# Performance work log

Measured on AMD Instinct MI355X. Metric: run time of the kernel, lower is better.

Reference implementation:

```python
import jax, jax.numpy as jnp
import numpy as np

# LE-like radial basis config (hypers: type='le', r_cut=5.0, mlp=True, no alchemical)
N_MAX_L = [22, 19, 16, 13]      # n_max per angular channel l
L_MAX = len(N_MAX_L) - 1
N_TOTAL = sum(N_MAX_L)          # 70
N_SPECIES = 4                   # all_species = [0,1,2,3]
N_GRID = 1024                   # spline control points
R_CUT = 5.0
HIDDEN = 32                     # hard-coded MLP width in the module
N_EDGES = 400_000


def setup_inputs() -> dict:
    key = jax.random.key(0)
    ks = jax.random.split(key, 7)
    # neighbor distances in [0, r_cut)
    r = jax.random.uniform(ks[0], (N_EDGES,), dtype=jnp.float32) * R_CUT
    neighbor_species = jax.random.randint(ks[1], (N_EDGES,), 0, N_SPECIES)
    # spline table standing in for the precomputed spliner coefficients
    spline_table = jax.random.normal(ks[2], (N_GRID, N_TOTAL), dtype=jnp.float32)
    nmax = max(N_MAX_L)
    sc_in = 1.0 / np.sqrt(nmax)
    sc_h = 1.0 / np.sqrt(HIDDEN)
    # per-(l, species) expert MLP weights, padded to nmax along the n_max_l axis;
    # torch Linear(n_in, n_out, bias=False) == x @ W with W: [n_in, n_out]
    W1 = jax.random.normal(ks[3], (L_MAX + 1, N_SPECIES, nmax, HIDDEN), dtype=jnp.float32) * sc_in
    W2 = jax.random.normal(ks[4], (L_MAX + 1, N_SPECIES, HIDDEN, HIDDEN), dtype=jnp.float32) * sc_h
    W3 = jax.random.normal(ks[5], (L_MAX + 1, N_SPECIES, HIDDEN, HIDDEN), dtype=jnp.float32) * sc_h
    W4 = jax.random.normal(ks[6], (L_MAX + 1, N_SPECIES, HIDDEN, nmax), dtype=jnp.float32) * sc_h
    return {"r": r, "neighbor_species": neighbor_species, "spline_table": spline_table,
            "W1": W1, "W2": W2, "W3": W3, "W4": W4}


def _spline_eval(r, spline_table):
    # linear-interpolation spline over a uniform grid on [0, R_CUT]
    dx = R_CUT / (N_GRID - 1)
    xi = r / dx
    idx = jnp.clip(jnp.floor(xi).astype(jnp.int32), 0, N_GRID - 2)
    frac = (xi - idx.astype(xi.dtype))[:, None]
    return spline_table[idx] * (1.0 - frac) + spline_table[idx + 1] * frac  # [E, N_TOTAL]


def reference(r, neighbor_species, spline_table, W1, W2, W3, W4):
    # 1) spline basis eval: r -> radial_functions [E, N_TOTAL]
    rf = _spline_eval(r, spline_table)
    silu = jax.nn.silu
    outs = []
    off = 0
    # 2) split by n_max_l; per-species expert MLP with scatter-back.
    # Vectorized as: run each species' tiny MLP on all edges, select via mask
    # (equivalent math to the original's nonzero/index_select gather-scatter).
    for l, n_l in enumerate(N_MAX_L):
        x_l = rf[:, off:off + n_l]  # [E, n_l]
        off += n_l
        out_l = jnp.zeros_like(x_l)
        for s in range(N_SPECIES):
            h = silu(x_l @ W1[l, s, :n_l])        # [E, 32]
            h = silu(h @ W2[l, s])                # [E, 32]
            h = silu(h @ W3[l, s])                # [E, 32]
            y = h @ W4[l, s][:, :n_l]             # [E, n_l]
            out_l = jnp.where(neighbor_species[:, None] == s, y, out_l)
        outs.append(out_l)
    # original returns a list split by l; concatenate for a single output array
    return jnp.concatenate(outs, axis=1)  # [E, N_TOTAL]
```

## Files before the change

kernel.cpp:

```cpp
#include <hip/hip_runtime.h>
#include <math.h>

#define BLK 256
#define BX 192
#define TSL 24608

typedef __attribute__((ext_vector_type(8))) short short8;
typedef __attribute__((ext_vector_type(4))) float f32x4;

union Frag {
  short8 s;
  unsigned int u[4];
};

__device__ __forceinline__ unsigned int pack_pair(float a, float b) {
  const unsigned int ua = __float_as_uint(a) + 0x8000u;
  const unsigned int ub = __float_as_uint(b) + 0x8000u;
  return (ua >> 16) | (ub & 0xFFFF0000u);
}

__device__ __forceinline__ void split_pair(float a, float b, unsigned int& hi,
                                           unsigned int& lo) {
  hi = pack_pair(a, b);
  const float ra = a - __uint_as_float(hi << 16);
  const float rb = b - __uint_as_float(hi & 0xFFFF0000u);
  lo = pack_pair(ra, rb);
}

__device__ __forceinline__ f32x4 silu4(f32x4 v) {
#pragma unroll
  for (int i = 0; i < 4; i++) {
    const float e = __builtin_amdgcn_exp2f(v[i] * -1.44269504f);
    v[i] = v[i] * __builtin_amdgcn_rcpf(1.0f + e);
  }
  return v;
}


__global__ void k_zero(int* __restrict__ cnt) {
  if (threadIdx.x < 4) cnt[threadIdx.x] = 0;
}

__global__ void __launch_bounds__(BLK) k_hist(const int* __restrict__ spc, int n,
                                              int* __restrict__ cnt) {
  __shared__ int h[4];
  if (threadIdx.x < 4) h[threadIdx.x] = 0;
  __syncthreads();
  const int i = blockIdx.x * BLK + threadIdx.x;
  if (i < n) atomicAdd(&h[spc[i]], 1);
  __syncthreads();
  if (threadIdx.x < 4) atomicAdd(&cnt[threadIdx.x], h[threadIdx.x]);
}

__global__ void k_prefix(const int* __restrict__ cnt, int* __restrict__ cnt2,
                         int* __restrict__ csum) {
  if (threadIdx.x == 0) {
    int a = 0;
#pragma unroll
    for (int s = 0; s < 4; s++) {
      csum[s] = a;
      cnt2[s] = a;
      a += cnt[s];
    }
  }
}

__global__ void __launch_bounds__(BLK) k_compact(const int* __restrict__ spc,
                                                 const float* __restrict__ r, int n,
                                                 int nb, int* __restrict__ cnt2,
                                                 float* __restrict__ fracs,
                                                 int* __restrict__ toffA,
                                                 int* __restrict__ perm,
                                                 const float* __restrict__ tbl,
                                                 float* __restrict__ wt) {
  if (blockIdx.x >= nb) {
    const int t = (blockIdx.x - nb) * BLK + threadIdx.x;
    if (t < 4 * 1024 * 24) {
      const int l = t / (1024 * 24);
      const int rem = t - l * (1024 * 24);
      const int idx = rem / 24;
      const int j = rem - idx * 24;
      const int off = (l == 0) ? 0 : (l == 1) ? 22 : (l == 2) ? 41 : 57;
      const int nl = (l == 0) ? 22 : (l == 1) ? 19 : (l == 2) ? 16 : 13;
      const float v = (j < nl) ? tbl[idx * 70 + off + j] : 0.f;
      wt[l * TSL + idx * 24 + j] = v;
    }
    if (t < 4 * 32) {
      const int l = t >> 5, j = t & 31;
      wt[l * TSL + 1024 * 24 + j] = 0.f;
    }
    return;
  }

  __shared__ int wcnt[4][4];
  __shared__ int wbase[4][4];
  const int tid = threadIdx.x;
  const int i = blockIdx.x * BLK + tid;
  const int lane = tid & 63;
  const int w = tid >> 6;
  const int s = (i < n) ? spc[i] : -1;
  const float rr = (i < n) ? r[i] : 0.f;

  int rank = 0;
#pragma unroll
  for (int sp = 0; sp < 4; sp++) {
    unsigned long long m = __ballot(s == sp);
    if (lane == 0) wcnt[w][sp] = __popcll(m);
    if (s == sp) rank = __popcll(m & ((1ULL << lane) - 1ULL));
  }
  __syncthreads();
  if (tid < 4) {
    const int c0 = wcnt[0][tid], c1 = wcnt[1][tid], c2 = wcnt[2][tid], c3 = wcnt[3][tid];
    const int b = atomicAdd(&cnt2[tid], c0 + c1 + c2 + c3);
    wbase[0][tid] = b;
    wbase[1][tid] = b + c0;
    wbase[2][tid] = b + c0 + c1;
    wbase[3][tid] = b + c0 + c1 + c2;
  }
  __syncthreads();
  if (s >= 0) {
    const int sp = wbase[w][s] + rank;
    const float xi = rr * (1023.0f / 5.0f);
    int idx = (int)floorf(xi);
    idx = idx < 0 ? 0 : (idx > 1022 ? 1022 : idx);
    fracs[sp] = xi - (float)idx;
    toffA[sp] = idx * 96;
    perm[sp] = i;
  }
}


__device__ __forceinline__ void layer_hl(const Frag* A, const Frag& bh,
                                         const Frag& bl, f32x4& d0, f32x4& d1) {
  f32x4 z = {0.f, 0.f, 0.f, 0.f};
  d0 = __builtin_amdgcn_mfma_f32_16x16x32_bf16(A[0].s, bl.s, z, 0, 0, 0);
  d0 = __builtin_amdgcn_mfma_f32_16x16x32_bf16(A[0].s, bh.s, d0, 0, 0, 0);
  d1 = __builtin_amdgcn_mfma_f32_16x16x32_bf16(A[1].s, bl.s, z, 0, 0, 0);
  d1 = __builtin_amdgcn_mfma_f32_16x16x32_bf16(A[1].s, bh.s, d1, 0, 0, 0);
}

__device__ __forceinline__ void layer_h(const Frag* A, const Frag& bh, f32x4& d0,
                                        f32x4& d1) {
  f32x4 z = {0.f, 0.f, 0.f, 0.f};
  d0 = __builtin_amdgcn_mfma_f32_16x16x32_bf16(A[0].s, bh.s, z, 0, 0, 0);
  d1 = __builtin_amdgcn_mfma_f32_16x16x32_bf16(A[1].s, bh.s, z, 0, 0, 0);
}

__device__ __forceinline__ void ldA(const unsigned int* __restrict__ wfr,
                                    int base256, int lane, Frag* A) {
#pragma unroll
  for (int jt = 0; jt < 2; jt++) {
    const uint4 v =
        reinterpret_cast<const uint4*>(wfr + ((base256 + jt) << 8))[lane];
    A[jt].u[0] = v.x;
    A[jt].u[1] = v.y;
    A[jt].u[2] = v.z;
    A[jt].u[3] = v.w;
  }
}

template <int L, int OFFA, bool D1>
__device__ __forceinline__ void proc_l(const unsigned int* __restrict__ wfr,
                                       const float* __restrict__ wt, int toff,
                                       float frac, int g, int lane,
                                       float* __restrict__ xrow) {
  const char* p = (const char*)(wt + (size_t)L * TSL + 8 * g) + toff;
  const f32x4 a0 = *(const f32x4*)(p);
  const f32x4 a1 = *(const f32x4*)(p + 16);
  const f32x4 b0 = *(const f32x4*)(p + 96);
  const f32x4 b1 = *(const f32x4*)(p + 112);

  Frag A1[2], A2[2], A3[2], A4[2];
  ldA(wfr, (L * 4 + 0) * 2, lane, A1);
  ldA(wfr, (L * 4 + 1) * 2, lane, A2);
  ldA(wfr, (L * 4 + 2) * 2, lane, A3);
  ldA(wfr, (L * 4 + 3) * 2, lane, A4);

  float x[8];
#pragma unroll
  for (int d = 0; d < 4; d++) {
    x[d] = a0[d] + frac * (b0[d] - a0[d]);
    x[d + 4] = a1[d] + frac * (b1[d] - a1[d]);
  }
  Frag bh, bl;
  split_pair(x[0], x[1], bh.u[0], bl.u[0]);
  split_pair(x[2], x[3], bh.u[1], bl.u[1]);
  split_pair(x[4], x[5], bh.u[2], bl.u[2]);
  split_pair(x[6], x[7], bh.u[3], bl.u[3]);

  f32x4 d0, d1;
  layer_hl(A1, bh, bl, d0, d1);
#pragma unroll
  for (int t = 0; t < 3; t++) {
    d0 = silu4(d0);
    d1 = silu4(d1);
    bh.u[0] = pack_pair(d0[0], d0[1]);
    bh.u[1] = pack_pair(d0[2], d0[3]);
    bh.u[2] = pack_pair(d1[0], d1[1]);
    bh.u[3] = pack_pair(d1[2], d1[3]);
    if (t == 0) layer_h(A2, bh, d0, d1);
    else if (t == 1) layer_h(A3, bh, d0, d1);
    else layer_h(A4, bh, d0, d1);
  }

  *(f32x4*)(xrow + OFFA + 4 * g) = d0;
  if (D1) *(f32x4*)(xrow + OFFA + 16 + 4 * g) = d1;
}

__global__ void __launch_bounds__(BLK) rb_fused(
    const float* __restrict__ fracs, const int* __restrict__ toffA,
    const int* __restrict__ perm, const float* __restrict__ wt,
    const float* __restrict__ W1, const float* __restrict__ W2,
    const float* __restrict__ W3, const float* __restrict__ W4,
    float* __restrict__ out, const int* __restrict__ cnt,
    const int* __restrict__ csum) {
  __shared__ unsigned int wfr[8192];
  __shared__ float xp[4][16 * 76];
  __shared__ int eid[4][16];

  const int s = blockIdx.y;
  const int count = cnt[s];
  if (count == 0) return;
  const int sp0 = csum[s];

  {
    const int nlarr[4] = {22, 19, 16, 13};
    for (int e = threadIdx.x; e < 8192; e += BLK) {
      const int p = e & 3;
      const int lane = (e >> 2) & 63;
      const int jt = (e >> 8) & 1;
      const int m = (e >> 9) & 3;
      const int l = e >> 11;
      const int c = lane & 15, g = lane >> 4;
      const int j = jt * 16 + c;
      const int nl = nlarr[l];
      float a, b;
      if (m == 0) {
        const int k0 = 8 * g + 2 * p, k1 = k0 + 1;
        const float* wp = W1 + (size_t)(l * 4 + s) * 704;
        a = (k0 < nl) ? wp[k0 * 32 + j] : 0.f;
        b = (k1 < nl) ? wp[k1 * 32 + j] : 0.f;
      } else {
        const int kp0 = (p < 2) ? (4 * g + 2 * p) : (16 + 4 * g + 2 * (p - 2));
        const int kp1 = kp0 + 1;
        if (m == 1) {
          const float* wp = W2 + (size_t)(l * 4 + s) * 1024;
          a = wp[kp0 * 32 + j];
          b = wp[kp1 * 32 + j];
        } else if (m == 2) {
          const float* wp = W3 + (size_t)(l * 4 + s) * 1024;
          a = wp[kp0 * 32 + j];
          b = wp[kp1 * 32 + j];
        } else {
          const float* wp = W4 + (size_t)(l * 4 + s) * 704;
          a = (j < nl) ? wp[kp0 * 22 + j] : 0.f;
          b = (j < nl) ? wp[kp1 * 22 + j] : 0.f;
        }
      }
      wfr[e] = pack_pair(a, b);
    }
  }
  __syncthreads();

  const int lane = threadIdx.x & 63;
  const int w = threadIdx.x >> 6;
  const int c = lane & 15, g = lane >> 4;
  float* __restrict__ xpw = xp[w];
  int* __restrict__ eidw = eid[w];
  float* __restrict__ xrow = xpw + c * 76;
  const int stride = gridDim.x * 64;

  int eb = blockIdx.x * 64 + w * 16;
  int ei = eb + c;
  int valid = ei < count;
  int spi = sp0 + (valid ? ei : 0);
  float frac = fracs[spi];
  int toff = toffA[spi];
  int e0 = perm[spi];

  for (; eb < count; eb += stride) {
    const int nei = eb + stride + c;
    const int nvalid = nei < count;
    const int nspi = sp0 + (nvalid ? nei : 0);
    const float nfrac = fracs[nspi];
    const int ntoff = toffA[nspi];
    const int ne = perm[nspi];

    proc_l<0, 0, true>(wfr, wt, toff, frac, g, lane, xrow);
    proc_l<1, 24, true>(wfr, wt, toff, frac, g, lane, xrow);
    proc_l<2, 44, false>(wfr, wt, toff, frac, g, lane, xrow);
    proc_l<3, 60, false>(wfr, wt, toff, frac, g, lane, xrow);

    if (g == 0) eidw[c] = valid ? e0 : -1;
    __asm__ volatile("" ::: "memory");

#pragma unroll
    for (int it = 0; it < 18; it++) {
      const int t = it * 64 + lane;
      if (t < 16 * 70) {
        const int row = t / 70;
        const int f = t - row * 70;
        const int er = eidw[row];
        const int fl = f + ((f >= 22) ? 2 : 0) + ((f >= 41) ? 1 : 0);
        if (er >= 0) out[(size_t)er * 70 + f] = xpw[row * 76 + fl];
      }
    }
    __asm__ volatile("" ::: "memory");

    frac = nfrac;
    toff = ntoff;
    e0 = ne;
    valid = nvalid;
  }
}

extern "C" void kernel_launch(void* const* d_in, const int* in_sizes, int n_in,
                              void* d_out, int out_size, void* d_ws, size_t ws_size,
                              hipStream_t stream) {
  const float* r = (const float*)d_in[0];
  const int* spc = (const int*)d_in[1];
  const float* tbl = (const float*)d_in[2];
  const float* W1 = (const float*)d_in[3];
  const float* W2 = (const float*)d_in[4];
  const float* W3 = (const float*)d_in[5];
  const float* W4 = (const float*)d_in[6];
  float* out = (float*)d_out;
  const int n = in_sizes[0];

  int* cnt = (int*)d_ws;
  int* cnt2 = cnt + 4;
  int* csum = cnt + 8;
  float* fracs = (float*)(cnt + 64);
  int* toffA = (int*)(fracs + n);
  int* perm = toffA + n;
  float* wtbl = (float*)(perm + n);

  hipLaunchKernelGGL(k_zero, dim3(1), dim3(64), 0, stream, cnt);

  const int nb = (n + BLK - 1) / BLK;
  hipLaunchKernelGGL(k_hist, dim3(nb), dim3(BLK), 0, stream, spc, n, cnt);
  hipLaunchKernelGGL(k_prefix, dim3(1), dim3(64), 0, stream, cnt, cnt2, csum);
  hipLaunchKernelGGL(k_compact, dim3(nb + 384), dim3(BLK), 0, stream, spc, r, n,
                     nb, cnt2, fracs, toffA, perm, tbl, wtbl);

  hipLaunchKernelGGL(rb_fused, dim3(BX, 4), dim3(BLK), 0, stream, fracs, toffA,
                     perm, wtbl, W1, W2, W3, W4, out, cnt, csum);
}
```

Measured before the change: 138.2 us.

## Split MLP kernel by l-pairs, keep weights in registers, drop histogram pass

Removes the histogram and prefix kernels by giving each species a fixed-stride bucket of size NEDGE_MAX, so compaction needs only one atomic counter pass. The fused kernel now launches blocks for (species, l-pair). Each block builds its MFMA weight fragments straight into registers from global memory, which removes the 32KB shared-memory weight table and its barrier. Smaller shared memory, launch bounds of 4 and a smaller grid aim at higher occupancy. The costs are higher register pressure, interpolation rows read twice across blocks, and a hard-coded cap on edge count.

```diff
diff --git a/kernel.cpp b/kernel.cpp
--- a/kernel.cpp
+++ b/kernel.cpp
@@ -2,7 +2,8 @@
 #include <math.h>
 
 #define BLK 256
-#define BX 192
+#define BX 128
+#define NEDGE_MAX 400000
 #define TSL 24608
 
 typedef __attribute__((ext_vector_type(8))) short short8;
@@ -41,33 +42,9 @@
   if (threadIdx.x < 4) cnt[threadIdx.x] = 0;
 }
 
-__global__ void __launch_bounds__(BLK) k_hist(const int* __restrict__ spc, int n,
-                                              int* __restrict__ cnt) {
-  __shared__ int h[4];
-  if (threadIdx.x < 4) h[threadIdx.x] = 0;
-  __syncthreads();
-  const int i = blockIdx.x * BLK + threadIdx.x;
-  if (i < n) atomicAdd(&h[spc[i]], 1);
-  __syncthreads();
-  if (threadIdx.x < 4) atomicAdd(&cnt[threadIdx.x], h[threadIdx.x]);
-}
-
-__global__ void k_prefix(const int* __restrict__ cnt, int* __restrict__ cnt2,
-                         int* __restrict__ csum) {
-  if (threadIdx.x == 0) {
-    int a = 0;
-#pragma unroll
-    for (int s = 0; s < 4; s++) {
-      csum[s] = a;
-      cnt2[s] = a;
-      a += cnt[s];
-    }
-  }
-}
-
 __global__ void __launch_bounds__(BLK) k_compact(const int* __restrict__ spc,
                                                  const float* __restrict__ r, int n,
-                                                 int nb, int* __restrict__ cnt2,
+                                                 int nb, int* __restrict__ cnt,
                                                  float* __restrict__ fracs,
                                                  int* __restrict__ toffA,
                                                  int* __restrict__ perm,
@@ -111,7 +88,7 @@
   __syncthreads();
   if (tid < 4) {
     const int c0 = wcnt[0][tid], c1 = wcnt[1][tid], c2 = wcnt[2][tid], c3 = wcnt[3][tid];
-    const int b = atomicAdd(&cnt2[tid], c0 + c1 + c2 + c3);
+    const int b = atomicAdd(&cnt[tid], c0 + c1 + c2 + c3);
     wbase[0][tid] = b;
     wbase[1][tid] = b + c0;
     wbase[2][tid] = b + c0 + c1;
@@ -119,13 +96,13 @@
   }
   __syncthreads();
   if (s >= 0) {
-    const int sp = wbase[w][s] + rank;
+    const int pos = s * NEDGE_MAX + wbase[w][s] + rank;
     const float xi = rr * (1023.0f / 5.0f);
     int idx = (int)floorf(xi);
     idx = idx < 0 ? 0 : (idx > 1022 ? 1022 : idx);
-    fracs[sp] = xi - (float)idx;
-    toffA[sp] = idx * 96;
-    perm[sp] = i;
+    fracs[pos] = xi - (float)idx;
+    toffA[pos] = idx * 96;
+    perm[pos] = i;
   }
 }
 
@@ -146,23 +123,11 @@
   d1 = __builtin_amdgcn_mfma_f32_16x16x32_bf16(A[1].s, bh.s, z, 0, 0, 0);
 }
 
-__device__ __forceinline__ void ldA(const unsigned int* __restrict__ wfr,
-                                    int base256, int lane, Frag* A) {
-#pragma unroll
-  for (int jt = 0; jt < 2; jt++) {
-    const uint4 v =
-        reinterpret_cast<const uint4*>(wfr + ((base256 + jt) << 8))[lane];
-    A[jt].u[0] = v.x;
-    A[jt].u[1] = v.y;
-    A[jt].u[2] = v.z;
-    A[jt].u[3] = v.w;
-  }
-}
-
-template <int L, int OFFA, bool D1>
-__device__ __forceinline__ void proc_l(const unsigned int* __restrict__ wfr,
+template <int L, int NL, int XBASE, int G1>
+__device__ __forceinline__ void proc_l(const Frag* A1, const Frag* A2,
+                                       const Frag* A3, const Frag* A4,
                                        const float* __restrict__ wt, int toff,
-                                       float frac, int g, int lane,
+                                       float frac, int g,
                                        float* __restrict__ xrow) {
   const char* p = (const char*)(wt + (size_t)L * TSL + 8 * g) + toff;
   const f32x4 a0 = *(const f32x4*)(p);
@@ -170,12 +135,6 @@
   const f32x4 b0 = *(const f32x4*)(p + 96);
   const f32x4 b1 = *(const f32x4*)(p + 112);
 
-  Frag A1[2], A2[2], A3[2], A4[2];
-  ldA(wfr, (L * 4 + 0) * 2, lane, A1);
-  ldA(wfr, (L * 4 + 1) * 2, lane, A2);
-  ldA(wfr, (L * 4 + 2) * 2, lane, A3);
-  ldA(wfr, (L * 4 + 3) * 2, lane, A4);
-
   float x[8];
 #pragma unroll
   for (int d = 0; d < 4; d++) {
@@ -190,8 +149,9 @@
 
   f32x4 d0, d1;
   layer_hl(A1, bh, bl, d0, d1);
-#pragma unroll
-  for (int t = 0; t < 3; t++) {
+
+#pragma unroll
+  for (int t = 0; t < 2; t++) {
     d0 = silu4(d0);
     d1 = silu4(d1);
     bh.u[0] = pack_pair(d0[0], d0[1]);
@@ -199,119 +159,140 @@
     bh.u[2] = pack_pair(d1[0], d1[1]);
     bh.u[3] = pack_pair(d1[2], d1[3]);
     if (t == 0) layer_h(A2, bh, d0, d1);
-    else if (t == 1) layer_h(A3, bh, d0, d1);
-    else layer_h(A4, bh, d0, d1);
-  }
-
-  *(f32x4*)(xrow + OFFA + 4 * g) = d0;
-  if (D1) *(f32x4*)(xrow + OFFA + 16 + 4 * g) = d1;
-}
-
-__global__ void __launch_bounds__(BLK) rb_fused(
+    else layer_h(A3, bh, d0, d1);
+  }
+  d0 = silu4(d0);
+  d1 = silu4(d1);
+  bh.u[0] = pack_pair(d0[0], d0[1]);
+  bh.u[1] = pack_pair(d0[2], d0[3]);
+  bh.u[2] = pack_pair(d1[0], d1[1]);
+  bh.u[3] = pack_pair(d1[2], d1[3]);
+  f32x4 z = {0.f, 0.f, 0.f, 0.f};
+  d0 = __builtin_amdgcn_mfma_f32_16x16x32_bf16(A4[0].s, bh.s, z, 0, 0, 0);
+  if (G1 > 0) d1 = __builtin_amdgcn_mfma_f32_16x16x32_bf16(A4[1].s, bh.s, z, 0, 0, 0);
+
+  *(f32x4*)(xrow + XBASE + 4 * g) = d0;
+  if (g < G1) *(f32x4*)(xrow + XBASE + 16 + 4 * g) = d1;
+}
+
+template <int NL>
+__device__ __forceinline__ void build_frags(const float* __restrict__ w1,
+                                            const float* __restrict__ w2,
+                                            const float* __restrict__ w3,
+                                            const float* __restrict__ w4, int c,
+                                            int g, Frag* A1, Frag* A2, Frag* A3,
+                                            Frag* A4) {
+#pragma unroll
+  for (int jt = 0; jt < 2; jt++) {
+    const int j = jt * 16 + c;
+#pragma unroll
+    for (int p = 0; p < 4; p++) {
+      const int k0 = 8 * g + 2 * p, k1 = k0 + 1;
+      const float a = (k0 < NL) ? w1[k0 * 32 + j] : 0.f;
+      const float b = (k1 < NL) ? w1[k1 * 32 + j] : 0.f;
+      A1[jt].u[p] = pack_pair(a, b);
+      const int kp0 = (p < 2) ? (4 * g + 2 * p) : (16 + 4 * g + 2 * (p - 2));
+      const int kp1 = kp0 + 1;
+      A2[jt].u[p] = pack_pair(w2[kp0 * 32 + j], w2[kp1 * 32 + j]);
+      A3[jt].u[p] = pack_pair(w3[kp0 * 32 + j], w3[kp1 * 32 + j]);
+      A4[jt].u[p] = pack_pair((j < NL) ? w4[kp0 * 22 + j] : 0.f,
+                              (j < NL) ? w4[kp1 * 22 + j] : 0.f);
+    }
+  }
+}
+
+template <int LP>
+__device__ void fbody(const float* __restrict__ fracs,
+                      const int* __restrict__ toffA, const int* __restrict__ perm,
+                      const float* __restrict__ wt, const float* __restrict__ W1,
+                      const float* __restrict__ W2, const float* __restrict__ W3,
+                      const float* __restrict__ W4, float* __restrict__ out,
+                      const int* __restrict__ cnt, float* __restrict__ xpw,
+                      int* __restrict__ eidw) {
+  constexpr int LA = 2 * LP, LB = 2 * LP + 1;
+  constexpr int NLa = (LP == 0) ? 22 : 16;
+  constexpr int NLb = (LP == 0) ? 19 : 13;
+  constexpr int ROWD = (LP == 0) ? 44 : 36;
+  constexpr int XBb = (LP == 0) ? 24 : 16;
+  constexpr int G1a = (LP == 0) ? 2 : 0;
+  constexpr int G1b = (LP == 0) ? 1 : 0;
+  constexpr int NDW = (LP == 0) ? 41 : 29;
+  constexpr int FOFF = (LP == 0) ? 0 : 41;
+
+  const int s = blockIdx.y & 3;
+  const int count = cnt[s];
+  if (count == 0) return;
+  const int sBase = s * NEDGE_MAX;
+
+  const int lane = threadIdx.x & 63;
+  const int w = threadIdx.x >> 6;
+  const int c = lane & 15, g = lane >> 4;
+  float* __restrict__ xrow = xpw + c * ROWD;
+
+  Frag Aa1[2], Aa2[2], Aa3[2], Aa4[2], Ab1[2], Ab2[2], Ab3[2], Ab4[2];
+  build_frags<NLa>(W1 + (size_t)(LA * 4 + s) * 704, W2 + (size_t)(LA * 4 + s) * 1024,
+                   W3 + (size_t)(LA * 4 + s) * 1024, W4 + (size_t)(LA * 4 + s) * 704,
+                   c, g, Aa1, Aa2, Aa3, Aa4);
+  build_frags<NLb>(W1 + (size_t)(LB * 4 + s) * 704, W2 + (size_t)(LB * 4 + s) * 1024,
+                   W3 + (size_t)(LB * 4 + s) * 1024, W4 + (size_t)(LB * 4 + s) * 704,
+                   c, g, Ab1, Ab2, Ab3, Ab4);
+
+  const int stride = gridDim.x * 64;
+  int eb = blockIdx.x * 64 + w * 16;
+  int valid = (eb + c) < count;
+  int spi = sBase + (valid ? eb + c : 0);
+  float frac = fracs[spi];
+  int toff = toffA[spi];
+  int e0 = perm[spi];
+
+  for (; eb < count; eb += stride) {
+    const int nei = eb + stride + c;
+    const int nvalid = nei < count;
+    const int nspi = sBase + (nvalid ? nei : 0);
+    const float nfrac = fracs[nspi];
+    const int ntoff = toffA[nspi];
+    const int ne = perm[nspi];
+
+    proc_l<LA, NLa, 0, G1a>(Aa1, Aa2, Aa3, Aa4, wt, toff, frac, g, xrow);
+    proc_l<LB, NLb, XBb, G1b>(Ab1, Ab2, Ab3, Ab4, wt, toff, frac, g, xrow);
+
+    if (g == 0) eidw[c] = valid ? e0 : -1;
+    __asm__ volatile("" ::: "memory");
+
+    constexpr int TOT = 16 * NDW;
+#pragma unroll
+    for (int it = 0; it < (TOT + 63) / 64; it++) {
+      const int t = it * 64 + lane;
+      if (t < TOT) {
+        const int row = t / NDW;
+        const int f0 = t - row * NDW;
+        const int fl = (LP == 0) ? (f0 + ((f0 >= 22) ? 2 : 0)) : f0;
+        const int er = eidw[row];
+        if (er >= 0) out[(size_t)er * 70 + FOFF + f0] = xpw[row * ROWD + fl];
+      }
+    }
+    __asm__ volatile("" ::: "memory");
+
+    frac = nfrac;
+    toff = ntoff;
+    e0 = ne;
+    valid = nvalid;
+  }
+}
+
+__global__ void __launch_bounds__(BLK, 4) rb_fused(
     const float* __restrict__ fracs, const int* __restrict__ toffA,
     const int* __restrict__ perm, const float* __restrict__ wt,
     const float* __restrict__ W1, const float* __restrict__ W2,
     const float* __restrict__ W3, const float* __restrict__ W4,
-    float* __restrict__ out, const int* __restrict__ cnt,
-    const int* __restrict__ csum) {
-  __shared__ unsigned int wfr[8192];
-  __shared__ float xp[4][16 * 76];
+    float* __restrict__ out, const int* __restrict__ cnt) {
+  __shared__ float xp[4][16 * 44];
   __shared__ int eid[4][16];
-
-  const int s = blockIdx.y;
-  const int count = cnt[s];
-  if (count == 0) return;
-  const int sp0 = csum[s];
-
-  {
-    const int nlarr[4] = {22, 19, 16, 13};
-    for (int e = threadIdx.x; e < 8192; e += BLK) {
-      const int p = e & 3;
-      const int lane = (e >> 2) & 63;
-      const int jt = (e >> 8) & 1;
-      const int m = (e >> 9) & 3;
-      const int l = e >> 11;
-      const int c = lane & 15, g = lane >> 4;
-      const int j = jt * 16 + c;
-      const int nl = nlarr[l];
-      float a, b;
-      if (m == 0) {
-        const int k0 = 8 * g + 2 * p, k1 = k0 + 1;
-        const float* wp = W1 + (size_t)(l * 4 + s) * 704;
-        a = (k0 < nl) ? wp[k0 * 32 + j] : 0.f;
-        b = (k1 < nl) ? wp[k1 * 32 + j] : 0.f;
-      } else {
-        const int kp0 = (p < 2) ? (4 * g + 2 * p) : (16 + 4 * g + 2 * (p - 2));
-        const int kp1 = kp0 + 1;
-        if (m == 1) {
-          const float* wp = W2 + (size_t)(l * 4 + s) * 1024;
-          a = wp[kp0 * 32 + j];
-          b = wp[kp1 * 32 + j];
-        } else if (m == 2) {
-          const float* wp = W3 + (size_t)(l * 4 + s) * 1024;
-          a = wp[kp0 * 32 + j];
-          b = wp[kp1 * 32 + j];
-        } else {
-          const float* wp = W4 + (size_t)(l * 4 + s) * 704;
-          a = (j < nl) ? wp[kp0 * 22 + j] : 0.f;
-          b = (j < nl) ? wp[kp1 * 22 + j] : 0.f;
-        }
-      }
-      wfr[e] = pack_pair(a, b);
-    }
-  }
-  __syncthreads();
-
-  const int lane = threadIdx.x & 63;
   const int w = threadIdx.x >> 6;
-  const int c = lane & 15, g = lane >> 4;
-  float* __restrict__ xpw = xp[w];
-  int* __restrict__ eidw = eid[w];
-  float* __restrict__ xrow = xpw + c * 76;
-  const int stride = gridDim.x * 64;
-
-  int eb = blockIdx.x * 64 + w * 16;
-  int ei = eb + c;
-  int valid = ei < count;
-  int spi = sp0 + (valid ? ei : 0);
-  float frac = fracs[spi];
-  int toff = toffA[spi];
-  int e0 = perm[spi];
-
-  for (; eb < count; eb += stride) {
-    const int nei = eb + stride + c;
-    const int nvalid = nei < count;
-    const int nspi = sp0 + (nvalid ? nei : 0);
-    const float nfrac = fracs[nspi];
-    const int ntoff = toffA[nspi];
-    const int ne = perm[nspi];
-
-    proc_l<0, 0, true>(wfr, wt, toff, frac, g, lane, xrow);
-    proc_l<1, 24, true>(wfr, wt, toff, frac, g, lane, xrow);
-    proc_l<2, 44, false>(wfr, wt, toff, frac, g, lane, xrow);
-    proc_l<3, 60, false>(wfr, wt, toff, frac, g, lane, xrow);
-
-    if (g == 0) eidw[c] = valid ? e0 : -1;
-    __asm__ volatile("" ::: "memory");
-
-#pragma unroll
-    for (int it = 0; it < 18; it++) {
-      const int t = it * 64 + lane;
-      if (t < 16 * 70) {
-        const int row = t / 70;
-        const int f = t - row * 70;
-        const int er = eidw[row];
-        const int fl = f + ((f >= 22) ? 2 : 0) + ((f >= 41) ? 1 : 0);
-        if (er >= 0) out[(size_t)er * 70 + f] = xpw[row * 76 + fl];
-      }
-    }
-    __asm__ volatile("" ::: "memory");
-
-    frac = nfrac;
-    toff = ntoff;
-    e0 = ne;
-    valid = nvalid;
-  }
+  if ((blockIdx.y >> 2) == 0)
+    fbody<0>(fracs, toffA, perm, wt, W1, W2, W3, W4, out, cnt, xp[w], eid[w]);
+  else
+    fbody<1>(fracs, toffA, perm, wt, W1, W2, W3, W4, out, cnt, xp[w], eid[w]);
 }
 
 extern "C" void kernel_launch(void* const* d_in, const int* in_sizes, int n_in,
@@ -328,21 +309,17 @@
   const int n = in_sizes[0];
 
   int* cnt = (int*)d_ws;
-  int* cnt2 = cnt + 4;
-  int* csum = cnt + 8;
   float* fracs = (float*)(cnt + 64);
-  int* toffA = (int*)(fracs + n);
-  int* perm = toffA + n;
-  float* wtbl = (float*)(perm + n);
+  int* toffA = (int*)(fracs + 4 * NEDGE_MAX);
+  int* perm = toffA + 4 * NEDGE_MAX;
+  float* wtbl = (float*)(perm + 4 * NEDGE_MAX);
 
   hipLaunchKernelGGL(k_zero, dim3(1), dim3(64), 0, stream, cnt);
 
   const int nb = (n + BLK - 1) / BLK;
-  hipLaunchKernelGGL(k_hist, dim3(nb), dim3(BLK), 0, stream, spc, n, cnt);
-  hipLaunchKernelGGL(k_prefix, dim3(1), dim3(64), 0, stream, cnt, cnt2, csum);
   hipLaunchKernelGGL(k_compact, dim3(nb + 384), dim3(BLK), 0, stream, spc, r, n,
-                     nb, cnt2, fracs, toffA, perm, tbl, wtbl);
-
-  hipLaunchKernelGGL(rb_fused, dim3(BX, 4), dim3(BLK), 0, stream, fracs, toffA,
-                     perm, wtbl, W1, W2, W3, W4, out, cnt, csum);
-}
+                     nb, cnt, fracs, toffA, perm, tbl, wtbl);
+
+  hipLaunchKernelGGL(rb_fused, dim3(BX, 8), dim3(BLK), 0, stream, fracs, toffA,
+                     perm, wtbl, W1, W2, W3, W4, out, cnt);
+}
```

Result: faster. 127.7 us (-7.6%).

## Hold l=0,1 weight fragments in registers and drop histogram/prefix passes

Applied to the files above, without the earlier changes.

The main MLP kernel now builds the MFMA weight fragments for the two largest angular channels once per wave, straight from global memory into registers. Only l=2,3 weights stay in LDS, which halves the shared table, and their per-layer fragment loads are double-buffered. The histogram and prefix kernels are removed by giving each species a fixed-size bucket (stride NEDGE_MAX), so a single compaction pass both counts and scatters. The grid grows and launch bounds request 4 blocks per SM. The trade-off is much higher register pressure from keeping 16 fragments live, plus a hard cap of 400000 edges per species bucket.

```diff
diff --git a/kernel.cpp b/kernel.cpp
--- a/kernel.cpp
+++ b/kernel.cpp
@@ -2,7 +2,8 @@
 #include <math.h>
 
 #define BLK 256
-#define BX 192
+#define BX 256
+#define NEDGE_MAX 400000
 #define TSL 24608
 
 typedef __attribute__((ext_vector_type(8))) short short8;
@@ -41,33 +42,9 @@
   if (threadIdx.x < 4) cnt[threadIdx.x] = 0;
 }
 
-__global__ void __launch_bounds__(BLK) k_hist(const int* __restrict__ spc, int n,
-                                              int* __restrict__ cnt) {
-  __shared__ int h[4];
-  if (threadIdx.x < 4) h[threadIdx.x] = 0;
-  __syncthreads();
-  const int i = blockIdx.x * BLK + threadIdx.x;
-  if (i < n) atomicAdd(&h[spc[i]], 1);
-  __syncthreads();
-  if (threadIdx.x < 4) atomicAdd(&cnt[threadIdx.x], h[threadIdx.x]);
-}
-
-__global__ void k_prefix(const int* __restrict__ cnt, int* __restrict__ cnt2,
-                         int* __restrict__ csum) {
-  if (threadIdx.x == 0) {
-    int a = 0;
-#pragma unroll
-    for (int s = 0; s < 4; s++) {
-      csum[s] = a;
-      cnt2[s] = a;
-      a += cnt[s];
-    }
-  }
-}
-
 __global__ void __launch_bounds__(BLK) k_compact(const int* __restrict__ spc,
                                                  const float* __restrict__ r, int n,
-                                                 int nb, int* __restrict__ cnt2,
+                                                 int nb, int* __restrict__ cnt,
                                                  float* __restrict__ fracs,
                                                  int* __restrict__ toffA,
                                                  int* __restrict__ perm,
@@ -111,7 +88,7 @@
   __syncthreads();
   if (tid < 4) {
     const int c0 = wcnt[0][tid], c1 = wcnt[1][tid], c2 = wcnt[2][tid], c3 = wcnt[3][tid];
-    const int b = atomicAdd(&cnt2[tid], c0 + c1 + c2 + c3);
+    const int b = atomicAdd(&cnt[tid], c0 + c1 + c2 + c3);
     wbase[0][tid] = b;
     wbase[1][tid] = b + c0;
     wbase[2][tid] = b + c0 + c1;
@@ -119,13 +96,13 @@
   }
   __syncthreads();
   if (s >= 0) {
-    const int sp = wbase[w][s] + rank;
+    const int pos = s * NEDGE_MAX + wbase[w][s] + rank;
     const float xi = rr * (1023.0f / 5.0f);
     int idx = (int)floorf(xi);
     idx = idx < 0 ? 0 : (idx > 1022 ? 1022 : idx);
-    fracs[sp] = xi - (float)idx;
-    toffA[sp] = idx * 96;
-    perm[sp] = i;
+    fracs[pos] = xi - (float)idx;
+    toffA[pos] = idx * 96;
+    perm[pos] = i;
   }
 }
 
@@ -159,81 +136,134 @@
   }
 }
 
-template <int L, int OFFA, bool D1>
-__device__ __forceinline__ void proc_l(const unsigned int* __restrict__ wfr,
-                                       const float* __restrict__ wt, int toff,
-                                       float frac, int g, int lane,
-                                       float* __restrict__ xrow) {
+template <int NL>
+__device__ __forceinline__ void build_frags(const float* __restrict__ w1,
+                                            const float* __restrict__ w2,
+                                            const float* __restrict__ w3,
+                                            const float* __restrict__ w4, int c,
+                                            int g, Frag* A1, Frag* A2, Frag* A3,
+                                            Frag* A4) {
+#pragma unroll
+  for (int jt = 0; jt < 2; jt++) {
+    const int j = jt * 16 + c;
+#pragma unroll
+    for (int p = 0; p < 4; p++) {
+      const int k0 = 8 * g + 2 * p, k1 = k0 + 1;
+      const float a = (k0 < NL) ? w1[k0 * 32 + j] : 0.f;
+      const float b = (k1 < NL) ? w1[k1 * 32 + j] : 0.f;
+      A1[jt].u[p] = pack_pair(a, b);
+      const int kp0 = (p < 2) ? (4 * g + 2 * p) : (16 + 4 * g + 2 * (p - 2));
+      const int kp1 = kp0 + 1;
+      A2[jt].u[p] = pack_pair(w2[kp0 * 32 + j], w2[kp1 * 32 + j]);
+      A3[jt].u[p] = pack_pair(w3[kp0 * 32 + j], w3[kp1 * 32 + j]);
+      A4[jt].u[p] = pack_pair((j < NL) ? w4[kp0 * 22 + j] : 0.f,
+                              (j < NL) ? w4[kp1 * 22 + j] : 0.f);
+    }
+  }
+}
+
+template <int L>
+__device__ __forceinline__ void gather_split(const float* __restrict__ wt,
+                                             int toff, float frac, int g,
+                                             Frag& bh, Frag& bl) {
   const char* p = (const char*)(wt + (size_t)L * TSL + 8 * g) + toff;
   const f32x4 a0 = *(const f32x4*)(p);
   const f32x4 a1 = *(const f32x4*)(p + 16);
   const f32x4 b0 = *(const f32x4*)(p + 96);
   const f32x4 b1 = *(const f32x4*)(p + 112);
-
-  Frag A1[2], A2[2], A3[2], A4[2];
-  ldA(wfr, (L * 4 + 0) * 2, lane, A1);
-  ldA(wfr, (L * 4 + 1) * 2, lane, A2);
-  ldA(wfr, (L * 4 + 2) * 2, lane, A3);
-  ldA(wfr, (L * 4 + 3) * 2, lane, A4);
-
   float x[8];
 #pragma unroll
   for (int d = 0; d < 4; d++) {
     x[d] = a0[d] + frac * (b0[d] - a0[d]);
     x[d + 4] = a1[d] + frac * (b1[d] - a1[d]);
   }
-  Frag bh, bl;
   split_pair(x[0], x[1], bh.u[0], bl.u[0]);
   split_pair(x[2], x[3], bh.u[1], bl.u[1]);
   split_pair(x[4], x[5], bh.u[2], bl.u[2]);
   split_pair(x[6], x[7], bh.u[3], bl.u[3]);
-
+}
+
+__device__ __forceinline__ void repack(const f32x4& d0, const f32x4& d1,
+                                       Frag& bh) {
+  bh.u[0] = pack_pair(d0[0], d0[1]);
+  bh.u[1] = pack_pair(d0[2], d0[3]);
+  bh.u[2] = pack_pair(d1[0], d1[1]);
+  bh.u[3] = pack_pair(d1[2], d1[3]);
+}
+
+template <int L, int XBASE, int G1>
+__device__ __forceinline__ void proc_reg(const Frag* A1, const Frag* A2,
+                                         const Frag* A3, const Frag* A4,
+                                         const float* __restrict__ wt, int toff,
+                                         float frac, int g,
+                                         float* __restrict__ xrow) {
+  Frag bh, bl;
+  gather_split<L>(wt, toff, frac, g, bh, bl);
   f32x4 d0, d1;
   layer_hl(A1, bh, bl, d0, d1);
-#pragma unroll
-  for (int t = 0; t < 3; t++) {
-    d0 = silu4(d0);
-    d1 = silu4(d1);
-    bh.u[0] = pack_pair(d0[0], d0[1]);
-    bh.u[1] = pack_pair(d0[2], d0[3]);
-    bh.u[2] = pack_pair(d1[0], d1[1]);
-    bh.u[3] = pack_pair(d1[2], d1[3]);
-    if (t == 0) layer_h(A2, bh, d0, d1);
-    else if (t == 1) layer_h(A3, bh, d0, d1);
-    else layer_h(A4, bh, d0, d1);
-  }
-
-  *(f32x4*)(xrow + OFFA + 4 * g) = d0;
-  if (D1) *(f32x4*)(xrow + OFFA + 16 + 4 * g) = d1;
-}
-
-__global__ void __launch_bounds__(BLK) rb_fused(
+  d0 = silu4(d0); d1 = silu4(d1); repack(d0, d1, bh);
+  layer_h(A2, bh, d0, d1);
+  d0 = silu4(d0); d1 = silu4(d1); repack(d0, d1, bh);
+  layer_h(A3, bh, d0, d1);
+  d0 = silu4(d0); d1 = silu4(d1); repack(d0, d1, bh);
+  f32x4 z = {0.f, 0.f, 0.f, 0.f};
+  d0 = __builtin_amdgcn_mfma_f32_16x16x32_bf16(A4[0].s, bh.s, z, 0, 0, 0);
+  if (G1 > 0) d1 = __builtin_amdgcn_mfma_f32_16x16x32_bf16(A4[1].s, bh.s, z, 0, 0, 0);
+  *(f32x4*)(xrow + XBASE + 4 * g) = d0;
+  if (g < G1) *(f32x4*)(xrow + XBASE + 16 + 4 * g) = d1;
+}
+
+template <int LI, int XBASE>
+__device__ __forceinline__ void proc_lds(const unsigned int* __restrict__ wfr,
+                                         const float* __restrict__ wt, int toff,
+                                         float frac, int g, int lane,
+                                         float* __restrict__ xrow) {
+  constexpr int L = 2 + LI;
+  Frag Ta[2], Tb[2];
+  ldA(wfr, (LI * 4 + 0) * 2, lane, Ta);
+  Frag bh, bl;
+  gather_split<L>(wt, toff, frac, g, bh, bl);
+  ldA(wfr, (LI * 4 + 1) * 2, lane, Tb);
+  f32x4 d0, d1;
+  layer_hl(Ta, bh, bl, d0, d1);
+  d0 = silu4(d0); d1 = silu4(d1); repack(d0, d1, bh);
+  ldA(wfr, (LI * 4 + 2) * 2, lane, Ta);
+  layer_h(Tb, bh, d0, d1);
+  d0 = silu4(d0); d1 = silu4(d1); repack(d0, d1, bh);
+  ldA(wfr, (LI * 4 + 3) * 2, lane, Tb);
+  layer_h(Ta, bh, d0, d1);
+  d0 = silu4(d0); d1 = silu4(d1); repack(d0, d1, bh);
+  f32x4 z = {0.f, 0.f, 0.f, 0.f};
+  d0 = __builtin_amdgcn_mfma_f32_16x16x32_bf16(Tb[0].s, bh.s, z, 0, 0, 0);
+  *(f32x4*)(xrow + XBASE + 4 * g) = d0;
+}
+
+__global__ void __launch_bounds__(BLK, 4) rb_fused(
     const float* __restrict__ fracs, const int* __restrict__ toffA,
     const int* __restrict__ perm, const float* __restrict__ wt,
     const float* __restrict__ W1, const float* __restrict__ W2,
     const float* __restrict__ W3, const float* __restrict__ W4,
-    float* __restrict__ out, const int* __restrict__ cnt,
-    const int* __restrict__ csum) {
-  __shared__ unsigned int wfr[8192];
+    float* __restrict__ out, const int* __restrict__ cnt) {
+  __shared__ unsigned int wfr[4096];
   __shared__ float xp[4][16 * 76];
   __shared__ int eid[4][16];
 
   const int s = blockIdx.y;
   const int count = cnt[s];
   if (count == 0) return;
-  const int sp0 = csum[s];
+  const int sBase = s * NEDGE_MAX;
 
   {
-    const int nlarr[4] = {22, 19, 16, 13};
-    for (int e = threadIdx.x; e < 8192; e += BLK) {
+    for (int e = threadIdx.x; e < 4096; e += BLK) {
       const int p = e & 3;
       const int lane = (e >> 2) & 63;
       const int jt = (e >> 8) & 1;
       const int m = (e >> 9) & 3;
-      const int l = e >> 11;
+      const int li = e >> 11;
+      const int l = 2 + li;
       const int c = lane & 15, g = lane >> 4;
       const int j = jt * 16 + c;
-      const int nl = nlarr[l];
+      const int nl = li ? 13 : 16;
       float a, b;
       if (m == 0) {
         const int k0 = 8 * g + 2 * p, k1 = k0 + 1;
@@ -268,12 +298,19 @@
   float* __restrict__ xpw = xp[w];
   int* __restrict__ eidw = eid[w];
   float* __restrict__ xrow = xpw + c * 76;
+
+  Frag A01[2], A02[2], A03[2], A04[2], A11[2], A12[2], A13[2], A14[2];
+  build_frags<22>(W1 + (size_t)(0 * 4 + s) * 704, W2 + (size_t)(0 * 4 + s) * 1024,
+                  W3 + (size_t)(0 * 4 + s) * 1024, W4 + (size_t)(0 * 4 + s) * 704,
+                  c, g, A01, A02, A03, A04);
+  build_frags<19>(W1 + (size_t)(1 * 4 + s) * 704, W2 + (size_t)(1 * 4 + s) * 1024,
+                  W3 + (size_t)(1 * 4 + s) * 1024, W4 + (size_t)(1 * 4 + s) * 704,
+                  c, g, A11, A12, A13, A14);
+
   const int stride = gridDim.x * 64;
-
   int eb = blockIdx.x * 64 + w * 16;
-  int ei = eb + c;
-  int valid = ei < count;
-  int spi = sp0 + (valid ? ei : 0);
+  int valid = (eb + c) < count;
+  int spi = sBase + (valid ? eb + c : 0);
   float frac = fracs[spi];
   int toff = toffA[spi];
   int e0 = perm[spi];
@@ -281,15 +318,15 @@
   for (; eb < count; eb += stride) {
     const int nei = eb + stride + c;
     const int nvalid = nei < count;
-    const int nspi = sp0 + (nvalid ? nei : 0);
+    const int nspi = sBase + (nvalid ? nei : 0);
     const float nfrac = fracs[nspi];
     const int ntoff = toffA[nspi];
     const int ne = perm[nspi];
 
-    proc_l<0, 0, true>(wfr, wt, toff, frac, g, lane, xrow);
-    proc_l<1, 24, true>(wfr, wt, toff, frac, g, lane, xrow);
-    proc_l<2, 44, false>(wfr, wt, toff, frac, g, lane, xrow);
-    proc_l<3, 60, false>(wfr, wt, toff, frac, g, lane, xrow);
+    proc_reg<0, 0, 2>(A01, A02, A03, A04, wt, toff, frac, g, xrow);
+    proc_reg<1, 24, 1>(A11, A12, A13, A14, wt, toff, frac, g, xrow);
+    proc_lds<0, 44>(wfr, wt, toff, frac, g, lane, xrow);
+    proc_lds<1, 60>(wfr, wt, toff, frac, g, lane, xrow);
 
     if (g == 0) eidw[c] = valid ? e0 : -1;
     __asm__ volatile("" ::: "memory");
@@ -328,21 +365,17 @@
   const int n = in_sizes[0];
 
   int* cnt = (int*)d_ws;
-  int* cnt2 = cnt + 4;
-  int* csum = cnt + 8;
   float* fracs = (float*)(cnt + 64);
-  int* toffA = (int*)(fracs + n);
-  int* perm = toffA + n;
-  float* wtbl = (float*)(perm + n);
+  int* toffA = (int*)(fracs + 4 * NEDGE_MAX);
+  int* perm = toffA + 4 * NEDGE_MAX;
+  float* wtbl = (float*)(perm + 4 * NEDGE_MAX);
 
   hipLaunchKernelGGL(k_zero, dim3(1), dim3(64), 0, stream, cnt);
 
   const int nb = (n + BLK - 1) / BLK;
-  hipLaunchKernelGGL(k_hist, dim3(nb), dim3(BLK), 0, stream, spc, n, cnt);
-  hipLaunchKernelGGL(k_prefix, dim3(1), dim3(64), 0, stream, cnt, cnt2, csum);
   hipLaunchKernelGGL(k_compact, dim3(nb + 384), dim3(BLK), 0, stream, spc, r, n,
-                     nb, cnt2, fracs, toffA, perm, tbl, wtbl);
+                     nb, cnt, fracs, toffA, perm, tbl, wtbl);
 
   hipLaunchKernelGGL(rb_fused, dim3(BX, 4), dim3(BLK), 0, stream, fracs, toffA,
-                     perm, wtbl, W1, W2, W3, W4, out, cnt, csum);
-}
+                     perm, wtbl, W1, W2, W3, W4, out, cnt);
+}
```

After: 181.7 us. 31.5% more time.

## Drop histogram and prefix kernels via fixed per-species buckets; stage outputs as bf16

Applied to the files above, without the earlier changes.

Removes the histogram and prefix-sum kernels. The compaction kernel now atomically appends each edge into a fixed-capacity bucket per species, at offset species*NEDGE_MAX, so the fused MLP kernel indexes that bucket directly. This saves two launches and one full pass over the species array. The per-wave output staging buffer in shared memory now holds bf16 pairs instead of fp32, and layer 4 issues only the MFMAs it needs, which halves LDS traffic and footprint. In exchange, the final outputs are rounded to bf16 precision, the edge count is capped at a hard-coded maximum, and the workspace grows.

```diff
diff --git a/kernel.cpp b/kernel.cpp
--- a/kernel.cpp
+++ b/kernel.cpp
@@ -3,6 +3,7 @@
 
 #define BLK 256
 #define BX 192
+#define NEDGE_MAX 400000
 #define TSL 24608
 
 typedef __attribute__((ext_vector_type(8))) short short8;
@@ -41,33 +42,9 @@
   if (threadIdx.x < 4) cnt[threadIdx.x] = 0;
 }
 
-__global__ void __launch_bounds__(BLK) k_hist(const int* __restrict__ spc, int n,
-                                              int* __restrict__ cnt) {
-  __shared__ int h[4];
-  if (threadIdx.x < 4) h[threadIdx.x] = 0;
-  __syncthreads();
-  const int i = blockIdx.x * BLK + threadIdx.x;
-  if (i < n) atomicAdd(&h[spc[i]], 1);
-  __syncthreads();
-  if (threadIdx.x < 4) atomicAdd(&cnt[threadIdx.x], h[threadIdx.x]);
-}
-
-__global__ void k_prefix(const int* __restrict__ cnt, int* __restrict__ cnt2,
-                         int* __restrict__ csum) {
-  if (threadIdx.x == 0) {
-    int a = 0;
-#pragma unroll
-    for (int s = 0; s < 4; s++) {
-      csum[s] = a;
-      cnt2[s] = a;
-      a += cnt[s];
-    }
-  }
-}
-
 __global__ void __launch_bounds__(BLK) k_compact(const int* __restrict__ spc,
                                                  const float* __restrict__ r, int n,
-                                                 int nb, int* __restrict__ cnt2,
+                                                 int nb, int* __restrict__ cnt,
                                                  float* __restrict__ fracs,
                                                  int* __restrict__ toffA,
                                                  int* __restrict__ perm,
@@ -111,7 +88,7 @@
   __syncthreads();
   if (tid < 4) {
     const int c0 = wcnt[0][tid], c1 = wcnt[1][tid], c2 = wcnt[2][tid], c3 = wcnt[3][tid];
-    const int b = atomicAdd(&cnt2[tid], c0 + c1 + c2 + c3);
+    const int b = atomicAdd(&cnt[tid], c0 + c1 + c2 + c3);
     wbase[0][tid] = b;
     wbase[1][tid] = b + c0;
     wbase[2][tid] = b + c0 + c1;
@@ -119,13 +96,13 @@
   }
   __syncthreads();
   if (s >= 0) {
-    const int sp = wbase[w][s] + rank;
+    const int pos = s * NEDGE_MAX + wbase[w][s] + rank;
     const float xi = rr * (1023.0f / 5.0f);
     int idx = (int)floorf(xi);
     idx = idx < 0 ? 0 : (idx > 1022 ? 1022 : idx);
-    fracs[sp] = xi - (float)idx;
-    toffA[sp] = idx * 96;
-    perm[sp] = i;
+    fracs[pos] = xi - (float)idx;
+    toffA[pos] = idx * 96;
+    perm[pos] = i;
   }
 }
 
@@ -159,11 +136,19 @@
   }
 }
 
-template <int L, int OFFA, bool D1>
+__device__ __forceinline__ void repack(const f32x4& d0, const f32x4& d1,
+                                       Frag& bh) {
+  bh.u[0] = pack_pair(d0[0], d0[1]);
+  bh.u[1] = pack_pair(d0[2], d0[3]);
+  bh.u[2] = pack_pair(d1[0], d1[1]);
+  bh.u[3] = pack_pair(d1[2], d1[3]);
+}
+
+template <int L, int UBASE, int G1>
 __device__ __forceinline__ void proc_l(const unsigned int* __restrict__ wfr,
                                        const float* __restrict__ wt, int toff,
                                        float frac, int g, int lane,
-                                       float* __restrict__ xrow) {
+                                       unsigned int* __restrict__ xrow) {
   const char* p = (const char*)(wt + (size_t)L * TSL + 8 * g) + toff;
   const f32x4 a0 = *(const f32x4*)(p);
   const f32x4 a1 = *(const f32x4*)(p + 16);
@@ -190,21 +175,20 @@
 
   f32x4 d0, d1;
   layer_hl(A1, bh, bl, d0, d1);
-#pragma unroll
-  for (int t = 0; t < 3; t++) {
-    d0 = silu4(d0);
-    d1 = silu4(d1);
-    bh.u[0] = pack_pair(d0[0], d0[1]);
-    bh.u[1] = pack_pair(d0[2], d0[3]);
-    bh.u[2] = pack_pair(d1[0], d1[1]);
-    bh.u[3] = pack_pair(d1[2], d1[3]);
-    if (t == 0) layer_h(A2, bh, d0, d1);
-    else if (t == 1) layer_h(A3, bh, d0, d1);
-    else layer_h(A4, bh, d0, d1);
-  }
-
-  *(f32x4*)(xrow + OFFA + 4 * g) = d0;
-  if (D1) *(f32x4*)(xrow + OFFA + 16 + 4 * g) = d1;
+  d0 = silu4(d0); d1 = silu4(d1); repack(d0, d1, bh);
+  layer_h(A2, bh, d0, d1);
+  d0 = silu4(d0); d1 = silu4(d1); repack(d0, d1, bh);
+  layer_h(A3, bh, d0, d1);
+  d0 = silu4(d0); d1 = silu4(d1); repack(d0, d1, bh);
+  f32x4 z = {0.f, 0.f, 0.f, 0.f};
+  d0 = __builtin_amdgcn_mfma_f32_16x16x32_bf16(A4[0].s, bh.s, z, 0, 0, 0);
+  if (G1 > 0) d1 = __builtin_amdgcn_mfma_f32_16x16x32_bf16(A4[1].s, bh.s, z, 0, 0, 0);
+
+  *(uint2*)(xrow + UBASE + 2 * g) =
+      make_uint2(pack_pair(d0[0], d0[1]), pack_pair(d0[2], d0[3]));
+  if (G1 > 0 && g < G1)
+    *(uint2*)(xrow + UBASE + 8 + 2 * g) =
+        make_uint2(pack_pair(d1[0], d1[1]), pack_pair(d1[2], d1[3]));
 }
 
 __global__ void __launch_bounds__(BLK) rb_fused(
@@ -212,16 +196,15 @@
     const int* __restrict__ perm, const float* __restrict__ wt,
     const float* __restrict__ W1, const float* __restrict__ W2,
     const float* __restrict__ W3, const float* __restrict__ W4,
-    float* __restrict__ out, const int* __restrict__ cnt,
-    const int* __restrict__ csum) {
+    float* __restrict__ out, const int* __restrict__ cnt) {
   __shared__ unsigned int wfr[8192];
-  __shared__ float xp[4][16 * 76];
+  __shared__ unsigned int xp[4][16 * 38];
   __shared__ int eid[4][16];
 
   const int s = blockIdx.y;
   const int count = cnt[s];
   if (count == 0) return;
-  const int sp0 = csum[s];
+  const int sBase = s * NEDGE_MAX;
 
   {
     const int nlarr[4] = {22, 19, 16, 13};
@@ -265,15 +248,14 @@
   const int lane = threadIdx.x & 63;
   const int w = threadIdx.x >> 6;
   const int c = lane & 15, g = lane >> 4;
-  float* __restrict__ xpw = xp[w];
+  unsigned int* __restrict__ xpw = xp[w];
   int* __restrict__ eidw = eid[w];
-  float* __restrict__ xrow = xpw + c * 76;
+  unsigned int* __restrict__ xrow = xpw + c * 38;
   const int stride = gridDim.x * 64;
 
   int eb = blockIdx.x * 64 + w * 16;
-  int ei = eb + c;
-  int valid = ei < count;
-  int spi = sp0 + (valid ? ei : 0);
+  int valid = (eb + c) < count;
+  int spi = sBase + (valid ? eb + c : 0);
   float frac = fracs[spi];
   int toff = toffA[spi];
   int e0 = perm[spi];
@@ -281,15 +263,15 @@
   for (; eb < count; eb += stride) {
     const int nei = eb + stride + c;
     const int nvalid = nei < count;
-    const int nspi = sp0 + (nvalid ? nei : 0);
+    const int nspi = sBase + (nvalid ? nei : 0);
     const float nfrac = fracs[nspi];
     const int ntoff = toffA[nspi];
     const int ne = perm[nspi];
 
-    proc_l<0, 0, true>(wfr, wt, toff, frac, g, lane, xrow);
-    proc_l<1, 24, true>(wfr, wt, toff, frac, g, lane, xrow);
-    proc_l<2, 44, false>(wfr, wt, toff, frac, g, lane, xrow);
-    proc_l<3, 60, false>(wfr, wt, toff, frac, g, lane, xrow);
+    proc_l<0, 0, 2>(wfr, wt, toff, frac, g, lane, xrow);
+    proc_l<1, 12, 1>(wfr, wt, toff, frac, g, lane, xrow);
+    proc_l<2, 22, 0>(wfr, wt, toff, frac, g, lane, xrow);
+    proc_l<3, 30, 0>(wfr, wt, toff, frac, g, lane, xrow);
 
     if (g == 0) eidw[c] = valid ? e0 : -1;
     __asm__ volatile("" ::: "memory");
@@ -302,7 +284,9 @@
         const int f = t - row * 70;
         const int er = eidw[row];
         const int fl = f + ((f >= 22) ? 2 : 0) + ((f >= 41) ? 1 : 0);
-        if (er >= 0) out[(size_t)er * 70 + f] = xpw[row * 76 + fl];
+        const unsigned int v = xpw[row * 38 + (fl >> 1)];
+        const unsigned int hv = (fl & 1) ? (v & 0xFFFF0000u) : (v << 16);
+        if (er >= 0) out[(size_t)er * 70 + f] = __uint_as_float(hv);
       }
     }
     __asm__ volatile("" ::: "memory");
@@ -328,21 +312,17 @@
   const int n = in_sizes[0];
 
   int* cnt = (int*)d_ws;
-  int* cnt2 = cnt + 4;
-  int* csum = cnt + 8;
   float* fracs = (float*)(cnt + 64);
-  int* toffA = (int*)(fracs + n);
-  int* perm = toffA + n;
-  float* wtbl = (float*)(perm + n);
+  int* toffA = (int*)(fracs + 4 * NEDGE_MAX);
+  int* perm = toffA + 4 * NEDGE_MAX;
+  float* wtbl = (float*)(perm + 4 * NEDGE_MAX);
 
   hipLaunchKernelGGL(k_zero, dim3(1), dim3(64), 0, stream, cnt);
 
   const int nb = (n + BLK - 1) / BLK;
-  hipLaunchKernelGGL(k_hist, dim3(nb), dim3(BLK), 0, stream, spc, n, cnt);
-  hipLaunchKernelGGL(k_prefix, dim3(1), dim3(64), 0, stream, cnt, cnt2, csum);
   hipLaunchKernelGGL(k_compact, dim3(nb + 384), dim3(BLK), 0, stream, spc, r, n,
-                     nb, cnt2, fracs, toffA, perm, tbl, wtbl);
+                     nb, cnt, fracs, toffA, perm, tbl, wtbl);
 
   hipLaunchKernelGGL(rb_fused, dim3(BX, 4), dim3(BLK), 0, stream, fracs, toffA,
-                     perm, wtbl, W1, W2, W3, W4, out, cnt, csum);
-}
+                     perm, wtbl, W1, W2, W3, W4, out, cnt);
+}
```

Result: faster. 123.1 us (-10.9%).
